# Kernel tuning notes

Hardware: AMD Instinct MI355X
Metric: run time of the kernel (lower is better)

## Reference

```python
import jax, jax.numpy as jnp
import numpy as np

B, D, H, DH = 2048, 1024, 8, 64  # batch, query_dim, heads, dim_head
INNER = H * DH  # 512


def setup_inputs() -> dict:
    key = jax.random.key(0)
    k0, k1, k2, k3 = jax.random.split(key, 4)
    x = jax.random.normal(k0, (B, D), dtype=jnp.float32)
    Wq = jax.random.normal(k1, (D, INNER), dtype=jnp.float32) * 0.02
    Wkv = jax.random.normal(k2, (D, 2 * INNER), dtype=jnp.float32) * 0.02
    Wout = jax.random.normal(k3, (INNER, D), dtype=jnp.float32) * 0.02
    bout = jnp.zeros((D,), dtype=jnp.float32)
    return {"x": x, "Wq": Wq, "Wkv": Wkv, "Wout": Wout, "bout": bout}


def reference(x, Wq, Wkv, Wout, bout):
    # Faithful to the original: 2D x, attention over the flattened (B*H) axis.
    b = x.shape[0]
    scale = DH ** -0.5
    q = (x @ Wq).reshape(b * H, DH)            # (b h) d
    k, v = jnp.split(x @ Wkv, 2, axis=-1)      # each [b, inner]
    k = k.reshape(b * H, DH)
    v = v.reshape(b * H, DH)
    sim = (q @ k.T) * scale                    # [(b h), (b h)] -- 1 GB intermediate
    attn = jax.nn.softmax(sim, axis=-1)        # dropout_rate = 0 -> identity
    out = (attn @ v).reshape(b, INNER)         # b (h d)
    return out @ Wout + bout                   # project_out path
```

## Files before the change

### kernel.cpp

```cpp
#include <hip/hip_runtime.h>
#include <hip/hip_bf16.h>
#include <stdint.h>


typedef __bf16 bf16_t;
typedef __bf16 bf16x4 __attribute__((ext_vector_type(4)));
typedef __bf16 bf16x8 __attribute__((ext_vector_type(8)));
typedef float floatx4 __attribute__((ext_vector_type(4)));

__device__ __forceinline__ floatx4 mfma16(bf16x8 a, bf16x8 b, floatx4 c) {
    return __builtin_amdgcn_mfma_f32_16x16x32_bf16(a, b, c, 0, 0, 0);
}

__device__ __forceinline__ bf16x8 cvt8(float4 a, float4 b) {
    bf16x8 o;
    o[0] = (bf16_t)a.x; o[1] = (bf16_t)a.y; o[2] = (bf16_t)a.z; o[3] = (bf16_t)a.w;
    o[4] = (bf16_t)b.x; o[5] = (bf16_t)b.y; o[6] = (bf16_t)b.z; o[7] = (bf16_t)b.w;
    return o;
}

__device__ __forceinline__ void transpose_body(const float* __restrict__ in, int N,
                                               bf16_t* __restrict__ out, int ldo,
                                               int bx, int by, int tid, float (*tile)[33]) {
    int n0 = bx * 32, k0 = by * 32;
    int tx = tid & 31, ty = tid >> 5;
#pragma unroll
    for (int i = 0; i < 32; i += 8)
        tile[ty + i][tx] = in[(size_t)(k0 + ty + i) * N + (n0 + tx)];
    __syncthreads();
#pragma unroll
    for (int i = 0; i < 32; i += 8)
        out[(size_t)(n0 + ty + i) * ldo + (k0 + tx)] = (bf16_t)tile[tx][ty + i];
}

__global__ __launch_bounds__(256) void prep_all(const float* __restrict__ x,
                                                bf16_t* __restrict__ xb,
                                                const float* __restrict__ Wq,
                                                const float* __restrict__ Wkv,
                                                const float* __restrict__ Wout,
                                                bf16_t* __restrict__ WtQKV,
                                                bf16_t* __restrict__ WtOut) {
    __shared__ float tile[32][33];
    int b = blockIdx.x, tid = threadIdx.x;
    if (b < 1024) {
        int i = (b * 256 + tid) * 8;
        *(bf16x8*)(xb + i) = cvt8(*(const float4*)(x + i), *(const float4*)(x + i + 4));
    } else if (b < 1536) {
        b -= 1024;
        transpose_body(Wq, 512, WtQKV, 1024, b & 15, b >> 4, tid, tile);
    } else if (b < 2560) {
        b -= 1536;
        transpose_body(Wkv, 1024, WtQKV + 512 * 1024, 1024, b & 31, b >> 5, tid, tile);
    } else {
        b -= 2560;
        transpose_body(Wout, 1024, WtOut, 512, b & 31, b >> 5, tid, tile);
    }
}

template <int OF32, int MI>
__global__ __launch_bounds__(256) void gemm_bt(const bf16_t* __restrict__ A,
                                               const bf16_t* __restrict__ Bt,
                                               const float* __restrict__ bias,
                                               void* __restrict__ Cout,
                                               bf16_t* __restrict__ VtOut, int vt_col0,
                                               int K, int lda, int ldb, int ldc,
                                               float qscale, int qcols) {
    constexpr int MT = MI * 32;
    constexpr int PA = MT / 64;
    __shared__ bf16_t sA[MT * 64];
    __shared__ bf16_t sB[64 * 64];
    int tid = threadIdx.x;
    int wave = tid >> 6, lane = tid & 63;
    int lm = lane & 15, q = lane >> 4;
    int bm = blockIdx.x * MT, bn = blockIdx.y * 64;
    int wm = (wave >> 1) * (MT / 2), wn = (wave & 1) * 32;

    int c0 = (tid & 3) * 2, c1 = c0 + 1;
    int rA[PA], swA[PA];
    size_t srcA0[PA], srcA1[PA];
#pragma unroll
    for (int p = 0; p < PA; ++p) {
        rA[p] = p * 64 + (tid >> 2);
        swA[p] = rA[p] & 7;
        srcA0[p] = (size_t)(bm + rA[p]) * lda + ((c0 ^ swA[p]) << 3);
        srcA1[p] = (size_t)(bm + rA[p]) * lda + ((c1 ^ swA[p]) << 3);
    }
    int rB = tid >> 2, swB = rB & 7;
    size_t srcB0 = (size_t)(bn + rB) * ldb + ((c0 ^ swB) << 3);
    size_t srcB1 = (size_t)(bn + rB) * ldb + ((c1 ^ swB) << 3);

    floatx4 acc[MI][2];
#pragma unroll
    for (int i = 0; i < MI; ++i)
#pragma unroll
        for (int j = 0; j < 2; ++j) acc[i][j] = (floatx4){0.f, 0.f, 0.f, 0.f};

    bf16x8 pa0[PA], pa1[PA], pb0, pb1;
#pragma unroll
    for (int p = 0; p < PA; ++p) {
        pa0[p] = *(const bf16x8*)(A + srcA0[p]);
        pa1[p] = *(const bf16x8*)(A + srcA1[p]);
    }
    pb0 = *(const bf16x8*)(Bt + srcB0);
    pb1 = *(const bf16x8*)(Bt + srcB1);
#pragma unroll
    for (int p = 0; p < PA; ++p) {
        *(bf16x8*)&sA[p * 4096 + tid * 16] = pa0[p];
        *(bf16x8*)&sA[p * 4096 + tid * 16 + 8] = pa1[p];
    }
    *(bf16x8*)&sB[tid * 16] = pb0;
    *(bf16x8*)&sB[tid * 16 + 8] = pb1;
    __syncthreads();

    for (int k0 = 0; k0 < K; k0 += 64) {
        int kn = (k0 + 64 < K) ? k0 + 64 : 0;
#pragma unroll
        for (int p = 0; p < PA; ++p) {
            pa0[p] = *(const bf16x8*)(A + srcA0[p] + kn);
            pa1[p] = *(const bf16x8*)(A + srcA1[p] + kn);
        }
        pb0 = *(const bf16x8*)(Bt + srcB0 + kn);
        pb1 = *(const bf16x8*)(Bt + srcB1 + kn);

#pragma unroll
        for (int s = 0; s < 2; ++s) {
            int cs = s * 4 + q;
            bf16x8 af[MI], bfr[2];
#pragma unroll
            for (int i = 0; i < MI; ++i) {
                int row = wm + i * 16 + lm;
                af[i] = *(bf16x8*)&sA[row * 64 + ((cs ^ (lm & 7)) << 3)];
            }
#pragma unroll
            for (int j = 0; j < 2; ++j) {
                int row = wn + j * 16 + lm;
                bfr[j] = *(bf16x8*)&sB[row * 64 + ((cs ^ (lm & 7)) << 3)];
            }
#pragma unroll
            for (int i = 0; i < MI; ++i)
#pragma unroll
                for (int j = 0; j < 2; ++j)
                    acc[i][j] = mfma16(af[i], bfr[j], acc[i][j]);
        }

        __syncthreads();
#pragma unroll
        for (int p = 0; p < PA; ++p) {
            *(bf16x8*)&sA[p * 4096 + tid * 16] = pa0[p];
            *(bf16x8*)&sA[p * 4096 + tid * 16 + 8] = pa1[p];
        }
        *(bf16x8*)&sB[tid * 16] = pb0;
        *(bf16x8*)&sB[tid * 16 + 8] = pb1;
        __syncthreads();
    }

#pragma unroll
    for (int i = 0; i < MI; ++i)
#pragma unroll
        for (int j = 0; j < 2; ++j)
#pragma unroll
            for (int r = 0; r < 4; ++r) {
                int row = bm + wm + i * 16 + q * 4 + r;
                int col = bn + wn + j * 16 + lm;
                float v = acc[i][j][r];
                if (col < qcols) v *= qscale;
                if (bias) v += bias[col];
                if (col >= vt_col0) {
                    int cc = col - vt_col0;
                    VtOut[(size_t)(cc & 63) * 16384 + row * 8 + (cc >> 6)] = (bf16_t)v;
                } else {
                    size_t off = (size_t)row * ldc + col;
                    if (OF32) ((float*)Cout)[off] = v;
                    else      ((bf16_t*)Cout)[off] = (bf16_t)v;
                }
            }
}

__global__ __launch_bounds__(256, 2) void flash_attn(const bf16_t* __restrict__ QK,
                                                     const bf16_t* __restrict__ Vt,
                                                     bf16_t* __restrict__ O,
                                                     float* __restrict__ accP,
                                                     float* __restrict__ lP,
                                                     int kps, int nsplit) {
    __shared__ bf16_t sK[64 * 64];
    __shared__ bf16_t sVt[64 * 64];
    __shared__ bf16_t sP[256 * 64];
    int tid = threadIdx.x;
    int wave = tid >> 6, lane = tid & 63;
    int lm = lane & 15, q = lane >> 4;
    int sp = blockIdx.y;
    int qrow0 = blockIdx.x * 256 + wave * 64;

    bf16x8 qf[4][2];
#pragma unroll
    for (int sub = 0; sub < 4; ++sub) {
        int qr = qrow0 + sub * 16 + lm;
        const bf16_t* qp = QK + (size_t)(qr >> 3) * 1024 + (qr & 7) * 64;
        qf[sub][0] = *(const bf16x8*)(qp + q * 8);
        qf[sub][1] = *(const bf16x8*)(qp + 32 + q * 8);
    }

    int sr = tid >> 2;
    int ch0 = (tid & 3) * 2, ch1 = ch0 + 1;
    int swz = sr & 7;
    int ksrcA = (sr >> 3) * 1024 + swz * 64 + 512 + ((ch0 ^ swz) << 3);
    int ksrcB = (sr >> 3) * 1024 + swz * 64 + 512 + ((ch1 ^ swz) << 3);
    size_t vsrcA = (size_t)sr * 16384 + ((ch0 ^ swz) << 3);
    size_t vsrcB = (size_t)sr * 16384 + ((ch1 ^ swz) << 3);
    bf16_t* dK = &sK[tid * 16];
    bf16_t* dV = &sVt[tid * 16];

    int c0 = q ^ (lm & 7);
    int rswz = (((lm >> 2) & 3) << 1) ^ ((lm >> 1) & 1);

    floatx4 acc[4][4];
#pragma unroll
    for (int sub = 0; sub < 4; ++sub)
#pragma unroll
        for (int i = 0; i < 4; ++i) acc[sub][i] = (floatx4){0.f, 0.f, 0.f, 0.f};
    float lacc[4][4];
#pragma unroll
    for (int sub = 0; sub < 4; ++sub)
#pragma unroll
        for (int r = 0; r < 4; ++r) lacc[sub][r] = 0.f;

    int kt0 = sp * kps, kend = kt0 + kps;

    bf16x8 krA, krB, vrA, vrB;
    {
        const bf16_t* kb = QK + (size_t)kt0 * 128;
        krA = *(const bf16x8*)(kb + ksrcA);
        krB = *(const bf16x8*)(kb + ksrcB);
        vrA = *(const bf16x8*)(Vt + vsrcA + kt0);
        vrB = *(const bf16x8*)(Vt + vsrcB + kt0);
    }
    *(bf16x8*)dK = krA; *(bf16x8*)(dK + 8) = krB;
    *(bf16x8*)dV = vrA; *(bf16x8*)(dV + 8) = vrB;
    __syncthreads();

    for (int kt = kt0; kt < kend; kt += 64) {
        int ktn = (kt + 64 < kend) ? kt + 64 : kt0;
        const bf16_t* kbn = QK + (size_t)ktn * 128;
        krA = *(const bf16x8*)(kbn + ksrcA);
        krB = *(const bf16x8*)(kbn + ksrcB);
        vrA = *(const bf16x8*)(Vt + vsrcA + ktn);
        vrB = *(const bf16x8*)(Vt + vsrcB + ktn);

#pragma unroll
        for (int nb = 0; nb < 4; ++nb) {
            int row = (nb * 16 + lm) * 64;
            bf16x8 k0 = *(bf16x8*)&sK[row + (c0 << 3)];
            bf16x8 k1 = *(bf16x8*)&sK[row + ((c0 ^ 4) << 3)];
#pragma unroll
            for (int sub = 0; sub < 4; ++sub) {
                floatx4 a = (floatx4){0.f, 0.f, 0.f, 0.f};
                a = mfma16(qf[sub][0], k0, a);
                a = mfma16(qf[sub][1], k1, a);
#pragma unroll
                for (int r = 0; r < 4; ++r) {
                    float pv = __builtin_amdgcn_exp2f(a[r]);
                    a[r] = pv;
                    lacc[sub][r] += pv;
                }
#pragma unroll
                for (int r2 = 0; r2 < 4; ++r2) {
                    int rowl = wave * 64 + sub * 16 + q * 4 + r2;
                    int col = nb * 16 + lm;
                    int kbs = (col >> 3) ^ (q << 1) ^ (r2 >> 1);
                    sP[rowl * 64 + (kbs << 3) + (col & 7)] = (bf16_t)a[r2];
                }
            }
        }

#pragma unroll
        for (int jb = 0; jb < 2; ++jb) {
            bf16x8 bv[4];
#pragma unroll
            for (int nd = 0; nd < 4; ++nd)
                bv[nd] = *(bf16x8*)&sVt[(nd * 16 + lm) * 64 + ((c0 ^ (jb << 2)) << 3)];
#pragma unroll
            for (int sub = 0; sub < 4; ++sub) {
                int rowr = wave * 64 + sub * 16 + lm;
                bf16x8 ap = *(bf16x8*)&sP[rowr * 64 + (((jb * 4 + q) ^ rswz) << 3)];
#pragma unroll
                for (int nd = 0; nd < 4; ++nd)
                    acc[sub][nd] = mfma16(ap, bv[nd], acc[sub][nd]);
            }
        }

        __syncthreads();
        *(bf16x8*)dK = krA; *(bf16x8*)(dK + 8) = krB;
        *(bf16x8*)dV = vrA; *(bf16x8*)(dV + 8) = vrB;
        __syncthreads();
    }

#pragma unroll
    for (int sub = 0; sub < 4; ++sub)
#pragma unroll
        for (int r = 0; r < 4; ++r)
#pragma unroll
            for (int off = 1; off < 16; off <<= 1)
                lacc[sub][r] += __shfl_xor(lacc[sub][r], off);

    if (nsplit == 1) {
#pragma unroll
        for (int sub = 0; sub < 4; ++sub)
#pragma unroll
            for (int r = 0; r < 4; ++r) {
                float inv = 1.f / lacc[sub][r];
                int row = qrow0 + sub * 16 + q * 4 + r;
#pragma unroll
                for (int nd = 0; nd < 4; ++nd)
                    O[(size_t)row * 64 + nd * 16 + lm] = (bf16_t)(acc[sub][nd][r] * inv);
            }
    } else {
#pragma unroll
        for (int sub = 0; sub < 4; ++sub)
#pragma unroll
            for (int r = 0; r < 4; ++r) {
                int row = qrow0 + sub * 16 + q * 4 + r;
                size_t base = ((size_t)sp * 16384 + row) * 64;
#pragma unroll
                for (int nd = 0; nd < 4; ++nd)
                    accP[base + nd * 16 + lm] = acc[sub][nd][r];
                if (lm == 0) lP[sp * 16384 + row] = lacc[sub][r];
            }
    }
}

__global__ __launch_bounds__(256) void merge_attn(const float* __restrict__ accP,
                                                  const float* __restrict__ lP,
                                                  bf16_t* __restrict__ O, int nsplit) {
    int idx = blockIdx.x * 256 + threadIdx.x;
    int row = idx >> 4, dh4 = (idx & 15) * 4;
    float4 num = {0.f, 0.f, 0.f, 0.f};
    float den = 0.f;
    for (int s = 0; s < nsplit; ++s) {
        float4 a = *(const float4*)&accP[((size_t)s * 16384 + row) * 64 + dh4];
        num.x += a.x; num.y += a.y; num.z += a.z; num.w += a.w;
        den += lP[s * 16384 + row];
    }
    float inv = 1.f / den;
    bf16x4 o;
    o[0] = (bf16_t)(num.x * inv); o[1] = (bf16_t)(num.y * inv);
    o[2] = (bf16_t)(num.z * inv); o[3] = (bf16_t)(num.w * inv);
    *(bf16x4*)&O[(size_t)row * 64 + dh4] = o;
}

extern "C" void kernel_launch(void* const* d_in, const int* in_sizes, int n_in,
                              void* d_out, int out_size, void* d_ws, size_t ws_size,
                              hipStream_t stream) {
    const float* x    = (const float*)d_in[0];
    const float* Wq   = (const float*)d_in[1];
    const float* Wkv  = (const float*)d_in[2];
    const float* Wout = (const float*)d_in[3];
    const float* bout = (const float*)d_in[4];

    char* ws = (char*)d_ws;
    bf16_t* QK    = (bf16_t*)ws;
    bf16_t* Vt    = (bf16_t*)(ws + 4194304);
    bf16_t* Ob    = (bf16_t*)(ws + 6291456);
    bf16_t* xb    = (bf16_t*)(ws + 8388608);
    bf16_t* WtQKV = (bf16_t*)(ws + 12582912);
    bf16_t* WtOut = (bf16_t*)(ws + 15728640);
    float*  accP  = (float*)(ws + 16777216);

    int nsplit = (ws_size >= (size_t)16777216 + 8 * 4259840) ? 8
               : (ws_size >= (size_t)16777216 + 4 * 4259840) ? 4
               : (ws_size >= (size_t)16777216 + 2 * 4259840) ? 2 : 1;
    float* lP = (float*)(ws + 16777216 + (size_t)nsplit * 4194304);

    prep_all<<<3072, 256, 0, stream>>>(x, xb, Wq, Wkv, Wout, WtQKV, WtOut);

    gemm_bt<0, 2><<<dim3(32, 24), 256, 0, stream>>>(
        xb, WtQKV, nullptr, QK, Vt, 1024, 1024, 1024, 1024, 1024,
        0.18033688011112042f, 512);

    flash_attn<<<dim3(64, nsplit), 256, 0, stream>>>(QK, Vt, Ob, accP, lP,
                                                     16384 / nsplit, nsplit);
    if (nsplit > 1)
        merge_attn<<<1024, 256, 0, stream>>>(accP, lP, Ob, nsplit);

    gemm_bt<1, 2><<<dim3(32, 16), 256, 0, stream>>>(
        Ob, WtOut, bout, d_out, nullptr, 1 << 30, 512, 512, 512, 1024,
        1.0f, 0);
}
```

Measured before the change: 198.3 us.

## Keep softmax probabilities in registers via transposed MFMA, removing LDS P staging

Computes S^T by swapping MFMA operands so each lane holds probabilities in the layout the PV MFMA's B operand needs. P is then packed to bf16 in registers instead of being written to and read back from a 32KB shared buffer. K rows are loaded with a permuted order so columns line up. Row sums now need only two cross-lane shuffles, and the output stores are vectorized. This cuts LDS traffic and footprint, which may help occupancy, at the cost of more live registers for the s/pf arrays.

```diff
diff --git a/kernel.cpp b/kernel.cpp
--- a/kernel.cpp
+++ b/kernel.cpp
@@ -184,7 +184,6 @@
                                                      int kps, int nsplit) {
     __shared__ bf16_t sK[64 * 64];
     __shared__ bf16_t sVt[64 * 64];
-    __shared__ bf16_t sP[256 * 64];
     int tid = threadIdx.x;
     int wave = tid >> 6, lane = tid & 63;
     int lm = lane & 15, q = lane >> 4;
@@ -203,26 +202,22 @@
     int sr = tid >> 2;
     int ch0 = (tid & 3) * 2, ch1 = ch0 + 1;
     int swz = sr & 7;
-    int ksrcA = (sr >> 3) * 1024 + swz * 64 + 512 + ((ch0 ^ swz) << 3);
-    int ksrcB = (sr >> 3) * 1024 + swz * 64 + 512 + ((ch1 ^ swz) << 3);
+    int lsr = 32 * (sr >> 5) + 8 * ((sr >> 2) & 3) + 4 * ((sr >> 4) & 1) + (sr & 3);
+    int ksrcA = (lsr >> 3) * 1024 + (lsr & 7) * 64 + 512 + ((ch0 ^ swz) << 3);
+    int ksrcB = (lsr >> 3) * 1024 + (lsr & 7) * 64 + 512 + ((ch1 ^ swz) << 3);
     size_t vsrcA = (size_t)sr * 16384 + ((ch0 ^ swz) << 3);
     size_t vsrcB = (size_t)sr * 16384 + ((ch1 ^ swz) << 3);
     bf16_t* dK = &sK[tid * 16];
     bf16_t* dV = &sVt[tid * 16];
 
     int c0 = q ^ (lm & 7);
-    int rswz = (((lm >> 2) & 3) << 1) ^ ((lm >> 1) & 1);
 
     floatx4 acc[4][4];
 #pragma unroll
     for (int sub = 0; sub < 4; ++sub)
 #pragma unroll
         for (int i = 0; i < 4; ++i) acc[sub][i] = (floatx4){0.f, 0.f, 0.f, 0.f};
-    float lacc[4][4];
-#pragma unroll
-    for (int sub = 0; sub < 4; ++sub)
-#pragma unroll
-        for (int r = 0; r < 4; ++r) lacc[sub][r] = 0.f;
+    float lacc[4] = {0.f, 0.f, 0.f, 0.f};
 
     int kt0 = sp * kps, kend = kt0 + kps;
 
@@ -246,6 +241,7 @@
         vrA = *(const bf16x8*)(Vt + vsrcA + ktn);
         vrB = *(const bf16x8*)(Vt + vsrcB + ktn);
 
+        floatx4 s[4][4];
 #pragma unroll
         for (int nb = 0; nb < 4; ++nb) {
             int row = (nb * 16 + lm) * 64;
@@ -254,38 +250,46 @@
 #pragma unroll
             for (int sub = 0; sub < 4; ++sub) {
                 floatx4 a = (floatx4){0.f, 0.f, 0.f, 0.f};
-                a = mfma16(qf[sub][0], k0, a);
-                a = mfma16(qf[sub][1], k1, a);
+                a = mfma16(k0, qf[sub][0], a);
+                a = mfma16(k1, qf[sub][1], a);
+                s[sub][nb] = a;
+            }
+        }
+
+        bf16x8 pf[4][2];
+#pragma unroll
+        for (int sub = 0; sub < 4; ++sub) {
+#pragma unroll
+            for (int nb = 0; nb < 4; ++nb)
 #pragma unroll
                 for (int r = 0; r < 4; ++r) {
-                    float pv = __builtin_amdgcn_exp2f(a[r]);
-                    a[r] = pv;
-                    lacc[sub][r] += pv;
+                    float pv = __builtin_amdgcn_exp2f(s[sub][nb][r]);
+                    s[sub][nb][r] = pv;
+                    lacc[sub] += pv;
                 }
 #pragma unroll
-                for (int r2 = 0; r2 < 4; ++r2) {
-                    int rowl = wave * 64 + sub * 16 + q * 4 + r2;
-                    int col = nb * 16 + lm;
-                    int kbs = (col >> 3) ^ (q << 1) ^ (r2 >> 1);
-                    sP[rowl * 64 + (kbs << 3) + (col & 7)] = (bf16_t)a[r2];
+            for (int jb = 0; jb < 2; ++jb) {
+                bf16x8 p;
+#pragma unroll
+                for (int r = 0; r < 4; ++r) {
+                    p[r] = (bf16_t)s[sub][2 * jb][r];
+                    p[r + 4] = (bf16_t)s[sub][2 * jb + 1][r];
                 }
+                pf[sub][jb] = p;
             }
         }
 
 #pragma unroll
         for (int jb = 0; jb < 2; ++jb) {
-            bf16x8 bv[4];
+            bf16x8 av[4];
 #pragma unroll
             for (int nd = 0; nd < 4; ++nd)
-                bv[nd] = *(bf16x8*)&sVt[(nd * 16 + lm) * 64 + ((c0 ^ (jb << 2)) << 3)];
-#pragma unroll
-            for (int sub = 0; sub < 4; ++sub) {
-                int rowr = wave * 64 + sub * 16 + lm;
-                bf16x8 ap = *(bf16x8*)&sP[rowr * 64 + (((jb * 4 + q) ^ rswz) << 3)];
+                av[nd] = *(bf16x8*)&sVt[(nd * 16 + lm) * 64 + ((c0 ^ (jb << 2)) << 3)];
+#pragma unroll
+            for (int sub = 0; sub < 4; ++sub)
 #pragma unroll
                 for (int nd = 0; nd < 4; ++nd)
-                    acc[sub][nd] = mfma16(ap, bv[nd], acc[sub][nd]);
-            }
+                    acc[sub][nd] = mfma16(av[nd], pf[sub][jb], acc[sub][nd]);
         }
 
         __syncthreads();
@@ -295,36 +299,37 @@
     }
 
 #pragma unroll
-    for (int sub = 0; sub < 4; ++sub)
-#pragma unroll
-        for (int r = 0; r < 4; ++r)
-#pragma unroll
-            for (int off = 1; off < 16; off <<= 1)
-                lacc[sub][r] += __shfl_xor(lacc[sub][r], off);
+    for (int sub = 0; sub < 4; ++sub) {
+        lacc[sub] += __shfl_xor(lacc[sub], 16);
+        lacc[sub] += __shfl_xor(lacc[sub], 32);
+    }
 
     if (nsplit == 1) {
 #pragma unroll
-        for (int sub = 0; sub < 4; ++sub)
-#pragma unroll
-            for (int r = 0; r < 4; ++r) {
-                float inv = 1.f / lacc[sub][r];
-                int row = qrow0 + sub * 16 + q * 4 + r;
-#pragma unroll
-                for (int nd = 0; nd < 4; ++nd)
-                    O[(size_t)row * 64 + nd * 16 + lm] = (bf16_t)(acc[sub][nd][r] * inv);
-            }
+        for (int sub = 0; sub < 4; ++sub) {
+            float inv = 1.f / lacc[sub];
+            int row = qrow0 + sub * 16 + lm;
+#pragma unroll
+            for (int nd = 0; nd < 4; ++nd) {
+                bf16x4 o;
+#pragma unroll
+                for (int r = 0; r < 4; ++r) o[r] = (bf16_t)(acc[sub][nd][r] * inv);
+                *(bf16x4*)&O[(size_t)row * 64 + nd * 16 + q * 4] = o;
+            }
+        }
     } else {
 #pragma unroll
-        for (int sub = 0; sub < 4; ++sub)
-#pragma unroll
-            for (int r = 0; r < 4; ++r) {
-                int row = qrow0 + sub * 16 + q * 4 + r;
-                size_t base = ((size_t)sp * 16384 + row) * 64;
-#pragma unroll
-                for (int nd = 0; nd < 4; ++nd)
-                    accP[base + nd * 16 + lm] = acc[sub][nd][r];
-                if (lm == 0) lP[sp * 16384 + row] = lacc[sub][r];
-            }
+        for (int sub = 0; sub < 4; ++sub) {
+            int row = qrow0 + sub * 16 + lm;
+            size_t base = ((size_t)sp * 16384 + row) * 64;
+#pragma unroll
+            for (int nd = 0; nd < 4; ++nd) {
+                float4 v = {acc[sub][nd][0], acc[sub][nd][1],
+                            acc[sub][nd][2], acc[sub][nd][3]};
+                *(float4*)&accP[base + nd * 16 + q * 4] = v;
+            }
+            if (lane < 16) lP[sp * 16384 + row] = lacc[sub];
+        }
     }
 }
 
```

Result: faster. 171.3 us (-13.6%).
